# Kernel optimization log

Hardware: AMD Instinct MI355X
Metric: run time of the kernel (lower is better)

## Reference

```python
import jax, jax.numpy as jnp
import numpy as np

EMBED_DIM = 1024
NUM_HEADS = 16
HEAD_DIM = EMBED_DIM // NUM_HEADS  # 64, == n_wires of quantum kernel


def setup_inputs() -> dict:
    key = jax.random.key(0)
    k1, k2, k3, k4 = jax.random.split(key, 4)
    B, S = 2, 2048
    x = jax.random.normal(k1, (B, S, EMBED_DIM), dtype=jnp.float32)
    # fused QKV projection (no bias); PyTorch Linear stores [out, in]
    qkv_w = jax.random.normal(k2, (3 * EMBED_DIM, EMBED_DIM), dtype=jnp.float32) / np.sqrt(EMBED_DIM)
    out_w = jax.random.normal(k3, (EMBED_DIM, EMBED_DIM), dtype=jnp.float32) / np.sqrt(EMBED_DIM)
    # one trainable RY angle per wire (shared across q, k, v and all heads)
    qparams = jax.random.normal(k4, (HEAD_DIM,), dtype=jnp.float32)
    return {"x": x, "qkv_w": qkv_w, "out_w": out_w, "qparams": qparams}


def _split_heads(t):
    B, S, E = t.shape
    return t.reshape(B, S, NUM_HEADS, HEAD_DIM).transpose(0, 2, 1, 3)  # [B,H,S,D]


def _apply_quantum(t, qparams):
    # RX(x_i)|0> then RY(p_i), measure <Z> on each wire independently:
    # <Z> = cos(x_i) * cos(p_i) -- separable single-qubit circuit reduces to trig.
    return jnp.cos(t) * jnp.cos(qparams)  # broadcast over last dim D


def reference(x, qkv_w, out_w, qparams):
    B, S, E = x.shape
    proj = x @ qkv_w.T                       # [B,S,3E]
    q, k, v = jnp.split(proj, 3, axis=-1)    # each [B,S,E]
    q = _apply_quantum(_split_heads(q), qparams)  # [B,H,S,D]
    k = _apply_quantum(_split_heads(k), qparams)
    v = _apply_quantum(_split_heads(v), qparams)
    scores = jnp.einsum('bhqd,bhkd->bhqk', q, k) / np.sqrt(HEAD_DIM)
    attn = jax.nn.softmax(scores, axis=-1)   # dropout is identity in eval
    out = jnp.einsum('bhqk,bhkd->bhqd', attn, v)  # [B,H,S,D]
    out = out.transpose(0, 2, 1, 3).reshape(B, S, E)
    return out @ out_w.T
```

## Files before the change

kernel.cpp:

```cpp
#include <hip/hip_runtime.h>
#include <hip/hip_bf16.h>

#define S_LEN 2048
#define EMB 1024
#define NH 16
#define HD 64

typedef __attribute__((ext_vector_type(8))) __bf16 bf16x8;
typedef __attribute__((ext_vector_type(4))) float f32x4;
typedef __attribute__((ext_vector_type(16))) float f32x16;
typedef __attribute__((ext_vector_type(4))) unsigned int u32x4;

__device__ inline void gload_lds16(const void* g, void* l) {
    __builtin_amdgcn_global_load_lds(
        (const __attribute__((address_space(1))) unsigned int*)g,
        (__attribute__((address_space(3))) unsigned int*)l, 16, 0, 0);
}

__global__ __launch_bounds__(256) void cvt_all(
    const float* __restrict__ x, const float* __restrict__ wq,
    const float* __restrict__ wo,
    __hip_bfloat16* __restrict__ xb, __hip_bfloat16* __restrict__ wqb,
    __hip_bfloat16* __restrict__ wob)
{
    const long C_X = (long)4096 * 1024 / 4;
    const long C_WQ = (long)3072 * 1024 / 4;
    long c = (long)blockIdx.x * 256 + threadIdx.x;
    const float* in;
    __hip_bfloat16* out;
    if (c < C_X) { in = x; out = xb; }
    else if (c < C_X + C_WQ) { in = wq; out = wqb; c -= C_X; }
    else { in = wo; out = wob; c -= C_X + C_WQ; }
    long i = c * 4;
    float4 v = *(const float4*)(in + i);
    __hip_bfloat16 b0 = __float2bfloat16(v.x);
    __hip_bfloat16 b1 = __float2bfloat16(v.y);
    __hip_bfloat16 b2 = __float2bfloat16(v.z);
    __hip_bfloat16 b3 = __float2bfloat16(v.w);
    ushort4 o = {*(unsigned short*)&b0, *(unsigned short*)&b1,
                 *(unsigned short*)&b2, *(unsigned short*)&b3};
    *(ushort4*)(out + i) = o;
}

template <int EPI>
__global__ __launch_bounds__(256) void gemm_mfma(
    const __hip_bfloat16* __restrict__ A,
    const __hip_bfloat16* __restrict__ B,
    const float* __restrict__ qp,
    __hip_bfloat16* __restrict__ Q,
    __hip_bfloat16* __restrict__ Kp,
    __hip_bfloat16* __restrict__ Vt,
    float* __restrict__ C)
{
    const int Kd = 1024;
    __shared__ __align__(16) char Ash[128 * 128];
    __shared__ __align__(16) char Bsh[128 * 128];

    const int t  = threadIdx.x;
    const int w  = t >> 6;
    const int l  = t & 63;
    const int lg = l >> 4, lm = l & 15;
    const int wr = w >> 1, wc = w & 1;
    const int m0 = blockIdx.y * 128;
    const int n0 = blockIdx.x * 128;

    const int r8 = l >> 3;
    const int sb = ((l & 7) * 16) ^ (r8 << 4);
    const char* srcA = (const char*)A + ((long)(m0 + w * 32 + r8) * Kd) * 2 + sb;
    const char* srcB = (const char*)B + ((long)(n0 + w * 32 + r8) * Kd) * 2 + sb;

    f32x4 acc[4][4];
#pragma unroll
    for (int i = 0; i < 4; i++)
#pragma unroll
        for (int j = 0; j < 4; j++) acc[i][j] = (f32x4){0.f, 0.f, 0.f, 0.f};

    for (int kt = 0; kt < Kd * 2; kt += 128) {
#pragma unroll
        for (int j = 0; j < 4; j++) {
            gload_lds16(srcA + (long)j * 8 * Kd * 2 + kt, Ash + (w * 32 + j * 8) * 128);
            gload_lds16(srcB + (long)j * 8 * Kd * 2 + kt, Bsh + (w * 32 + j * 8) * 128);
        }
        __syncthreads();
#pragma unroll
        for (int kk = 0; kk < 2; kk++) {
            bf16x8 af[4], bfr[4];
            const int sw = (lm & 7) << 4;
            const int co = (kk * 64 + lg * 16);
#pragma unroll
            for (int mi = 0; mi < 4; mi++)
                af[mi] = *(const bf16x8*)(Ash + (wr * 64 + mi * 16 + lm) * 128 + (co ^ sw));
#pragma unroll
            for (int ni = 0; ni < 4; ni++)
                bfr[ni] = *(const bf16x8*)(Bsh + (wc * 64 + ni * 16 + lm) * 128 + (co ^ sw));
#pragma unroll
            for (int mi = 0; mi < 4; mi++)
#pragma unroll
                for (int ni = 0; ni < 4; ni++)
                    acc[mi][ni] = __builtin_amdgcn_mfma_f32_16x16x32_bf16(
                        af[mi], bfr[ni], acc[mi][ni], 0, 0, 0);
        }
        __syncthreads();
    }

    if constexpr (EPI == 0) {
        const int which = n0 >> 10;
        float cqp[4];
#pragma unroll
        for (int ni = 0; ni < 4; ni++)
            cqp[ni] = __cosf(qp[(wc * 64 + ni * 16 + lm) & 63]);

        if (which == 2) {
            char* T = (w < 2 ? Ash : Bsh) + (w & 1) * 8192;
#pragma unroll
            for (int mi = 0; mi < 4; mi++)
#pragma unroll
                for (int r = 0; r < 4; r++)
#pragma unroll
                    for (int ni = 0; ni < 4; ni++) {
                        int row = ni * 16 + lm;
                        int col = mi * 16 + lg * 4 + r;
                        float val = __cosf(acc[mi][ni][r]) * cqp[ni];
                        *(__hip_bfloat16*)(T + row * 128 +
                                           ((col * 2) ^ ((row & 7) << 4))) =
                            __float2bfloat16(val);
                    }
            const int h  = ((n0 & 1023) >> 6) + wc;
            const int bh = (m0 >> 11) * NH + h;
            const int sbase = (m0 & 2047) + wr * 64;
#pragma unroll
            for (int j = 0; j < 8; j++) {
                int c = j * 64 + l;
                int d = c >> 3;
                int sc = (c & 7) * 16;
                uint4 v = *(const uint4*)(T + d * 128 + (sc ^ ((d & 7) << 4)));
                *(uint4*)((char*)(Vt + ((long)bh * HD + d) * S_LEN + sbase) + sc) = v;
            }
        } else {
#pragma unroll
            for (int mi = 0; mi < 4; mi++) {
#pragma unroll
                for (int r = 0; r < 4; r++) {
                    int m = m0 + wr * 64 + mi * 16 + lg * 4 + r;
                    int b = m >> 11, s = m & 2047;
#pragma unroll
                    for (int ni = 0; ni < 4; ni++) {
                        int n = n0 + wc * 64 + ni * 16 + lm;
                        int d = n & 63;
                        int h = (n & 1023) >> 6;
                        int bh = b * NH + h;
                        float val = __cosf(acc[mi][ni][r]) * cqp[ni];
                        if (which == 0)
                            Q[((long)bh * S_LEN + s) * HD + d] =
                                __float2bfloat16(val * 0.180336880f);
                        else
                            Kp[((long)bh * S_LEN + s) * HD + d] = __float2bfloat16(val);
                    }
                }
            }
        }
    } else {
#pragma unroll
        for (int mi = 0; mi < 4; mi++)
#pragma unroll
            for (int r = 0; r < 4; r++) {
                int m = m0 + wr * 64 + mi * 16 + lg * 4 + r;
#pragma unroll
                for (int ni = 0; ni < 4; ni++) {
                    int n = n0 + wc * 64 + ni * 16 + lm;
                    C[(long)m * 1024 + n] = acc[mi][ni][r];
                }
            }
    }
}

__global__ __launch_bounds__(256, 4) void attn_mfma(
    const __hip_bfloat16* __restrict__ Q,
    const __hip_bfloat16* __restrict__ K,
    const __hip_bfloat16* __restrict__ Vt,
    __hip_bfloat16* __restrict__ O)
{
    __shared__ __align__(16) char Ksh[2][64 * 128];
    __shared__ __align__(16) char Vsh[2][64 * 128];

    const int L  = blockIdx.x;
    const int bh = (L & 7) + (L >> 8) * 8;
    const int q0 = ((L >> 3) & 31) * 64;
    const int b  = bh >> 4, h = bh & 15;
    const int t  = threadIdx.x;
    const int w  = t >> 6;
    const int qi = w & 1;
    const int ki = w >> 1;
    const int l  = t & 63;
    const int lo5 = l & 31;
    const int hi  = l >> 5;

    const char* Qr =
        (const char*)(Q + ((long)bh * S_LEN + q0 + qi * 32 + lo5) * HD);
    bf16x8 qf[4];
#pragma unroll
    for (int ks = 0; ks < 4; ks++)
        qf[ks] = *(const bf16x8*)(Qr + ks * 32 + hi * 16);

    f32x16 oacc[2] = {};
    float lsum = 0.f;
    const float EXPB = 11.54156033f;

    const char* Kgb = (const char*)(K + (long)bh * S_LEN * HD);
    const char* Vgb = (const char*)(Vt + (long)bh * HD * S_LEN);

    const int swb = ((l & 7) * 16) ^ (((l >> 3) & 7) << 4);
    const int row0 = w * 8 + (l >> 3);
    const char* Ksrc  = Kgb + (long)row0 * 128 + swb;
    const char* Vsrc0 = Vgb + (long)row0 * (S_LEN * 2) + swb;
    const char* Vsrc1 = Vgb + (long)(row0 + 32) * (S_LEN * 2) + swb;

    gload_lds16(Ksrc, Ksh[0] + w * 1024);
    gload_lds16(Ksrc + 32 * 128, Ksh[0] + w * 1024 + 4096);
    gload_lds16(Vsrc0, Vsh[0] + w * 1024);
    gload_lds16(Vsrc1, Vsh[0] + w * 1024 + 4096);

    const int swr = (lo5 & 7) << 4;
    int cur = 0;
    for (int kt = 0; kt < S_LEN; kt += 64) {
        __syncthreads();

        if (kt + 64 < S_LEN) {
            int nk = kt + 64;
            gload_lds16(Ksrc + (long)nk * 128, Ksh[cur ^ 1] + w * 1024);
            gload_lds16(Ksrc + (long)(nk + 32) * 128, Ksh[cur ^ 1] + w * 1024 + 4096);
            gload_lds16(Vsrc0 + (long)nk * 2, Vsh[cur ^ 1] + w * 1024);
            gload_lds16(Vsrc1 + (long)nk * 2, Vsh[cur ^ 1] + w * 1024 + 4096);
        }

        const char* Kc = Ksh[cur];
        const char* Vc = Vsh[cur];

        f32x16 s;
#pragma unroll
        for (int r = 0; r < 16; r++) s[r] = -EXPB;
        const char* Krow = Kc + (ki * 32 + lo5) * 128;
        __builtin_amdgcn_s_setprio(1);
#pragma unroll
        for (int ks = 0; ks < 4; ks++) {
            bf16x8 kf = *(const bf16x8*)(Krow + ((ks * 32 + hi * 16) ^ swr));
            s = __builtin_amdgcn_mfma_f32_32x32x16_bf16(kf, qf[ks], s, 0, 0, 0);
        }
        __builtin_amdgcn_s_setprio(0);

        float p[16];
#pragma unroll
        for (int r = 0; r < 16; r++) p[r] = __builtin_amdgcn_exp2f(s[r]);
#pragma unroll
        for (int r = 0; r < 16; r += 4)
            lsum += (p[r] + p[r + 1]) + (p[r + 2] + p[r + 3]);
        unsigned c0, c1, c2, c3, c4, c5, c6, c7;
        asm("v_cvt_pk_bf16_f32 %0, %1, %2" : "=v"(c0) : "v"(p[0]),  "v"(p[1]));
        asm("v_cvt_pk_bf16_f32 %0, %1, %2" : "=v"(c1) : "v"(p[2]),  "v"(p[3]));
        asm("v_cvt_pk_bf16_f32 %0, %1, %2" : "=v"(c2) : "v"(p[4]),  "v"(p[5]));
        asm("v_cvt_pk_bf16_f32 %0, %1, %2" : "=v"(c3) : "v"(p[6]),  "v"(p[7]));
        asm("v_cvt_pk_bf16_f32 %0, %1, %2" : "=v"(c4) : "v"(p[8]),  "v"(p[9]));
        asm("v_cvt_pk_bf16_f32 %0, %1, %2" : "=v"(c5) : "v"(p[10]), "v"(p[11]));
        asm("v_cvt_pk_bf16_f32 %0, %1, %2" : "=v"(c6) : "v"(p[12]), "v"(p[13]));
        asm("v_cvt_pk_bf16_f32 %0, %1, %2" : "=v"(c7) : "v"(p[14]), "v"(p[15]));
        asm("v_permlane32_swap_b32 %0, %1" : "+v"(c0), "+v"(c2));
        asm("v_permlane32_swap_b32 %0, %1" : "+v"(c1), "+v"(c3));
        asm("v_permlane32_swap_b32 %0, %1" : "+v"(c4), "+v"(c6));
        asm("v_permlane32_swap_b32 %0, %1" : "+v"(c5), "+v"(c7));
        u32x4 w0 = {c0, c1, c2, c3};
        u32x4 w1 = {c4, c5, c6, c7};
        bf16x8 pa0 = __builtin_bit_cast(bf16x8, w0);
        bf16x8 pa1 = __builtin_bit_cast(bf16x8, w1);

        __builtin_amdgcn_s_setprio(1);
#pragma unroll
        for (int db = 0; db < 2; db++) {
            const char* Vrow = Vc + (db * 32 + lo5) * 128;
            bf16x8 vf0 = *(const bf16x8*)(Vrow + ((ki * 64 + hi * 16) ^ swr));
            bf16x8 vf1 = *(const bf16x8*)(Vrow + ((ki * 64 + 32 + hi * 16) ^ swr));
            oacc[db] = __builtin_amdgcn_mfma_f32_32x32x16_bf16(pa0, vf0, oacc[db], 0, 0, 0);
            oacc[db] = __builtin_amdgcn_mfma_f32_32x32x16_bf16(pa1, vf1, oacc[db], 0, 0, 0);
        }
        __builtin_amdgcn_s_setprio(0);
        cur ^= 1;
    }

    lsum += __shfl_xor(lsum, 32, 64);
    __syncthreads();
    float* Osh = (float*)Ksh;
    float* Lsh = (float*)Vsh;
    if (ki == 1) {
        float* dst = Osh + qi * 2048;
#pragma unroll
        for (int db = 0; db < 2; db++)
#pragma unroll
            for (int r = 0; r < 16; r++)
                dst[(db * 16 + r) * 64 + l] = oacc[db][r];
        Lsh[qi * 64 + l] = lsum;
    }
    __syncthreads();
    if (ki == 0) {
        const float* src = Osh + qi * 2048;
#pragma unroll
        for (int db = 0; db < 2; db++)
#pragma unroll
            for (int r = 0; r < 16; r++)
                oacc[db][r] += src[(db * 16 + r) * 64 + l];
        lsum += Lsh[qi * 64 + l];
        float inv = 1.f / lsum;
#pragma unroll
        for (int r = 0; r < 16; r++) {
            int qr = (r & 3) + 8 * (r >> 2) + 4 * hi;
            float invr = __shfl(inv, qr, 32);
            int qrow = q0 + qi * 32 + qr;
            long base = ((long)b * S_LEN + qrow) * EMB + h * HD;
            O[base + lo5]      = __float2bfloat16(oacc[0][r] * invr);
            O[base + 32 + lo5] = __float2bfloat16(oacc[1][r] * invr);
        }
    }
}

extern "C" void kernel_launch(void* const* d_in, const int* in_sizes, int n_in,
                              void* d_out, int out_size, void* d_ws, size_t ws_size,
                              hipStream_t stream) {
    const float* x     = (const float*)d_in[0];
    const float* qkv_w = (const float*)d_in[1];
    const float* out_w = (const float*)d_in[2];
    const float* qp    = (const float*)d_in[3];
    float* out = (float*)d_out;

    const long NELEM = (long)2 * S_LEN * EMB;
    __hip_bfloat16* Q   = (__hip_bfloat16*)d_ws;
    __hip_bfloat16* K   = Q + NELEM;
    __hip_bfloat16* Vt  = K + NELEM;
    __hip_bfloat16* O   = Vt + NELEM;
    __hip_bfloat16* xb  = O + NELEM;
    __hip_bfloat16* wqb = xb + NELEM;
    __hip_bfloat16* wob = wqb + (long)3072 * 1024;

    dim3 blk(256);
    cvt_all<<<dim3(8192), blk, 0, stream>>>(x, qkv_w, out_w, xb, wqb, wob);
    gemm_mfma<0><<<dim3(3072 / 128, 4096 / 128), blk, 0, stream>>>(
        xb, wqb, qp, Q, K, Vt, nullptr);
    attn_mfma<<<dim3(1024), blk, 0, stream>>>(Q, K, Vt, O);
    gemm_mfma<1><<<dim3(1024 / 128, 4096 / 128), blk, 0, stream>>>(
        O, wob, nullptr, nullptr, nullptr, nullptr, out);
}
```

Baseline: 118.0 us.

## Split attention KV across wave pairs and swizzle GEMM block order

```diff
diff --git a/kernel.cpp b/kernel.cpp
--- a/kernel.cpp
+++ b/kernel.cpp
@@ -42,7 +42,7 @@
     *(ushort4*)(out + i) = o;
 }
 
-template <int EPI>
+template <int EPI, int BN, int NX, int CH>
 __global__ __launch_bounds__(256) void gemm_mfma(
     const __hip_bfloat16* __restrict__ A,
     const __hip_bfloat16* __restrict__ B,
@@ -53,50 +53,56 @@
     float* __restrict__ C)
 {
     const int Kd = 1024;
+    const int NI = BN / 32;
     __shared__ __align__(16) char Ash[128 * 128];
-    __shared__ __align__(16) char Bsh[128 * 128];
+    __shared__ __align__(16) char Bsh[BN * 128];
+
+    const int bid = blockIdx.x;
+    const int sw_ = (bid & 7) * CH + (bid >> 3);
+    const int m0 = (sw_ / NX) * 128;
+    const int n0 = (sw_ % NX) * BN;
 
     const int t  = threadIdx.x;
     const int w  = t >> 6;
     const int l  = t & 63;
     const int lg = l >> 4, lm = l & 15;
     const int wr = w >> 1, wc = w & 1;
-    const int m0 = blockIdx.y * 128;
-    const int n0 = blockIdx.x * 128;
 
     const int r8 = l >> 3;
     const int sb = ((l & 7) * 16) ^ (r8 << 4);
     const char* srcA = (const char*)A + ((long)(m0 + w * 32 + r8) * Kd) * 2 + sb;
-    const char* srcB = (const char*)B + ((long)(n0 + w * 32 + r8) * Kd) * 2 + sb;
-
-    f32x4 acc[4][4];
+    const char* srcB = (const char*)B + ((long)(n0 + w * (BN / 4) + r8) * Kd) * 2 + sb;
+
+    f32x4 acc[4][NI];
 #pragma unroll
     for (int i = 0; i < 4; i++)
 #pragma unroll
-        for (int j = 0; j < 4; j++) acc[i][j] = (f32x4){0.f, 0.f, 0.f, 0.f};
+        for (int j = 0; j < NI; j++) acc[i][j] = (f32x4){0.f, 0.f, 0.f, 0.f};
 
     for (int kt = 0; kt < Kd * 2; kt += 128) {
 #pragma unroll
-        for (int j = 0; j < 4; j++) {
+        for (int j = 0; j < 4; j++)
             gload_lds16(srcA + (long)j * 8 * Kd * 2 + kt, Ash + (w * 32 + j * 8) * 128);
-            gload_lds16(srcB + (long)j * 8 * Kd * 2 + kt, Bsh + (w * 32 + j * 8) * 128);
-        }
+#pragma unroll
+        for (int j = 0; j < NI; j++)
+            gload_lds16(srcB + (long)j * 8 * Kd * 2 + kt,
+                        Bsh + (w * (BN / 4) + j * 8) * 128);
         __syncthreads();
 #pragma unroll
         for (int kk = 0; kk < 2; kk++) {
-            bf16x8 af[4], bfr[4];
+            bf16x8 af[4], bfr[NI];
             const int sw = (lm & 7) << 4;
             const int co = (kk * 64 + lg * 16);
 #pragma unroll
             for (int mi = 0; mi < 4; mi++)
                 af[mi] = *(const bf16x8*)(Ash + (wr * 64 + mi * 16 + lm) * 128 + (co ^ sw));
 #pragma unroll
-            for (int ni = 0; ni < 4; ni++)
-                bfr[ni] = *(const bf16x8*)(Bsh + (wc * 64 + ni * 16 + lm) * 128 + (co ^ sw));
+            for (int ni = 0; ni < NI; ni++)
+                bfr[ni] = *(const bf16x8*)(Bsh + (wc * (BN / 2) + ni * 16 + lm) * 128 + (co ^ sw));
 #pragma unroll
             for (int mi = 0; mi < 4; mi++)
 #pragma unroll
-                for (int ni = 0; ni < 4; ni++)
+                for (int ni = 0; ni < NI; ni++)
                     acc[mi][ni] = __builtin_amdgcn_mfma_f32_16x16x32_bf16(
                         af[mi], bfr[ni], acc[mi][ni], 0, 0, 0);
         }
@@ -105,10 +111,10 @@
 
     if constexpr (EPI == 0) {
         const int which = n0 >> 10;
-        float cqp[4];
-#pragma unroll
-        for (int ni = 0; ni < 4; ni++)
-            cqp[ni] = __cosf(qp[(wc * 64 + ni * 16 + lm) & 63]);
+        float cqp[NI];
+#pragma unroll
+        for (int ni = 0; ni < NI; ni++)
+            cqp[ni] = __cosf(qp[(wc * (BN / 2) + ni * 16 + lm) & 63]);
 
         if (which == 2) {
             char* T = (w < 2 ? Ash : Bsh) + (w & 1) * 8192;
@@ -117,7 +123,7 @@
 #pragma unroll
                 for (int r = 0; r < 4; r++)
 #pragma unroll
-                    for (int ni = 0; ni < 4; ni++) {
+                    for (int ni = 0; ni < NI; ni++) {
                         int row = ni * 16 + lm;
                         int col = mi * 16 + lg * 4 + r;
                         float val = __cosf(acc[mi][ni][r]) * cqp[ni];
@@ -144,8 +150,8 @@
                     int m = m0 + wr * 64 + mi * 16 + lg * 4 + r;
                     int b = m >> 11, s = m & 2047;
 #pragma unroll
-                    for (int ni = 0; ni < 4; ni++) {
-                        int n = n0 + wc * 64 + ni * 16 + lm;
+                    for (int ni = 0; ni < NI; ni++) {
+                        int n = n0 + wc * (BN / 2) + ni * 16 + lm;
                         int d = n & 63;
                         int h = (n & 1023) >> 6;
                         int bh = b * NH + h;
@@ -166,22 +172,21 @@
             for (int r = 0; r < 4; r++) {
                 int m = m0 + wr * 64 + mi * 16 + lg * 4 + r;
 #pragma unroll
-                for (int ni = 0; ni < 4; ni++) {
-                    int n = n0 + wc * 64 + ni * 16 + lm;
+                for (int ni = 0; ni < NI; ni++) {
+                    int n = n0 + wc * (BN / 2) + ni * 16 + lm;
                     C[(long)m * 1024 + n] = acc[mi][ni][r];
                 }
             }
     }
 }
 
-__global__ __launch_bounds__(256, 4) void attn_mfma(
+__global__ __launch_bounds__(256, 2) void attn_mfma(
     const __hip_bfloat16* __restrict__ Q,
     const __hip_bfloat16* __restrict__ K,
     const __hip_bfloat16* __restrict__ Vt,
     __hip_bfloat16* __restrict__ O)
 {
-    __shared__ __align__(16) char Ksh[2][64 * 128];
-    __shared__ __align__(16) char Vsh[2][64 * 128];
+    __shared__ __align__(16) char smem[65536 + 1024];
 
     const int L  = blockIdx.x;
     const int bh = (L & 7) + (L >> 8) * 8;
@@ -189,21 +194,22 @@
     const int b  = bh >> 4, h = bh & 15;
     const int t  = threadIdx.x;
     const int w  = t >> 6;
-    const int qi = w & 1;
-    const int ki = w >> 1;
+    const int sp = w >> 1, kh = w & 1;
     const int l  = t & 63;
     const int lo5 = l & 31;
     const int hi  = l >> 5;
 
-    const char* Qr =
-        (const char*)(Q + ((long)bh * S_LEN + q0 + qi * 32 + lo5) * HD);
-    bf16x8 qf[4];
-#pragma unroll
-    for (int ks = 0; ks < 4; ks++)
-        qf[ks] = *(const bf16x8*)(Qr + ks * 32 + hi * 16);
-
-    f32x16 oacc[2] = {};
-    float lsum = 0.f;
+    bf16x8 qf[2][4];
+#pragma unroll
+    for (int g = 0; g < 2; g++) {
+        const char* Qr = (const char*)(Q + ((long)bh * S_LEN + q0 + g * 32 + lo5) * HD);
+#pragma unroll
+        for (int ks = 0; ks < 4; ks++)
+            qf[g][ks] = *(const bf16x8*)(Qr + ks * 32 + hi * 16);
+    }
+
+    f32x16 oacc[2][2] = {};
+    float lsum[2] = {0.f, 0.f};
     const float EXPB = 11.54156033f;
 
     const char* Kgb = (const char*)(K + (long)bh * S_LEN * HD);
@@ -215,108 +221,116 @@
     const char* Vsrc0 = Vgb + (long)row0 * (S_LEN * 2) + swb;
     const char* Vsrc1 = Vgb + (long)(row0 + 32) * (S_LEN * 2) + swb;
 
-    gload_lds16(Ksrc, Ksh[0] + w * 1024);
-    gload_lds16(Ksrc + 32 * 128, Ksh[0] + w * 1024 + 4096);
-    gload_lds16(Vsrc0, Vsh[0] + w * 1024);
-    gload_lds16(Vsrc1, Vsh[0] + w * 1024 + 4096);
+#define STAGE(buf, nk)                                                         \
+    do {                                                                       \
+        _Pragma("unroll") for (int sp2 = 0; sp2 < 2; sp2++) {                  \
+            char* Kd_ = smem + ((buf) * 2 + sp2) * 8192;                       \
+            char* Vd_ = smem + 32768 + ((buf) * 2 + sp2) * 8192;               \
+            int kb = (nk) + sp2 * 64;                                          \
+            gload_lds16(Ksrc + (long)kb * 128, Kd_ + w * 1024);                \
+            gload_lds16(Ksrc + (long)(kb + 32) * 128, Kd_ + w * 1024 + 4096);  \
+            gload_lds16(Vsrc0 + (long)kb * 2, Vd_ + w * 1024);                 \
+            gload_lds16(Vsrc1 + (long)kb * 2, Vd_ + w * 1024 + 4096);          \
+        }                                                                      \
+    } while (0)
+
+    STAGE(0, 0);
 
     const int swr = (lo5 & 7) << 4;
     int cur = 0;
-    for (int kt = 0; kt < S_LEN; kt += 64) {
+    for (int rd = 0; rd < 16; rd++) {
         __syncthreads();
 
-        if (kt + 64 < S_LEN) {
-            int nk = kt + 64;
-            gload_lds16(Ksrc + (long)nk * 128, Ksh[cur ^ 1] + w * 1024);
-            gload_lds16(Ksrc + (long)(nk + 32) * 128, Ksh[cur ^ 1] + w * 1024 + 4096);
-            gload_lds16(Vsrc0 + (long)nk * 2, Vsh[cur ^ 1] + w * 1024);
-            gload_lds16(Vsrc1 + (long)nk * 2, Vsh[cur ^ 1] + w * 1024 + 4096);
-        }
-
-        const char* Kc = Ksh[cur];
-        const char* Vc = Vsh[cur];
-
-        f32x16 s;
-#pragma unroll
-        for (int r = 0; r < 16; r++) s[r] = -EXPB;
-        const char* Krow = Kc + (ki * 32 + lo5) * 128;
+        if (rd < 15) STAGE(cur ^ 1, (rd + 1) * 128);
+
+        const char* Kc = smem + (cur * 2 + sp) * 8192;
+        const char* Vc = smem + 32768 + (cur * 2 + sp) * 8192;
+
+        f32x16 s0, s1;
+#pragma unroll
+        for (int r = 0; r < 16; r++) { s0[r] = -EXPB; s1[r] = -EXPB; }
+        const char* Krow = Kc + (kh * 32 + lo5) * 128;
         __builtin_amdgcn_s_setprio(1);
 #pragma unroll
         for (int ks = 0; ks < 4; ks++) {
             bf16x8 kf = *(const bf16x8*)(Krow + ((ks * 32 + hi * 16) ^ swr));
-            s = __builtin_amdgcn_mfma_f32_32x32x16_bf16(kf, qf[ks], s, 0, 0, 0);
+            s0 = __builtin_amdgcn_mfma_f32_32x32x16_bf16(kf, qf[0][ks], s0, 0, 0, 0);
+            s1 = __builtin_amdgcn_mfma_f32_32x32x16_bf16(kf, qf[1][ks], s1, 0, 0, 0);
         }
         __builtin_amdgcn_s_setprio(0);
 
-        float p[16];
-#pragma unroll
-        for (int r = 0; r < 16; r++) p[r] = __builtin_amdgcn_exp2f(s[r]);
-#pragma unroll
-        for (int r = 0; r < 16; r += 4)
-            lsum += (p[r] + p[r + 1]) + (p[r + 2] + p[r + 3]);
-        unsigned c0, c1, c2, c3, c4, c5, c6, c7;
-        asm("v_cvt_pk_bf16_f32 %0, %1, %2" : "=v"(c0) : "v"(p[0]),  "v"(p[1]));
-        asm("v_cvt_pk_bf16_f32 %0, %1, %2" : "=v"(c1) : "v"(p[2]),  "v"(p[3]));
-        asm("v_cvt_pk_bf16_f32 %0, %1, %2" : "=v"(c2) : "v"(p[4]),  "v"(p[5]));
-        asm("v_cvt_pk_bf16_f32 %0, %1, %2" : "=v"(c3) : "v"(p[6]),  "v"(p[7]));
-        asm("v_cvt_pk_bf16_f32 %0, %1, %2" : "=v"(c4) : "v"(p[8]),  "v"(p[9]));
-        asm("v_cvt_pk_bf16_f32 %0, %1, %2" : "=v"(c5) : "v"(p[10]), "v"(p[11]));
-        asm("v_cvt_pk_bf16_f32 %0, %1, %2" : "=v"(c6) : "v"(p[12]), "v"(p[13]));
-        asm("v_cvt_pk_bf16_f32 %0, %1, %2" : "=v"(c7) : "v"(p[14]), "v"(p[15]));
-        asm("v_permlane32_swap_b32 %0, %1" : "+v"(c0), "+v"(c2));
-        asm("v_permlane32_swap_b32 %0, %1" : "+v"(c1), "+v"(c3));
-        asm("v_permlane32_swap_b32 %0, %1" : "+v"(c4), "+v"(c6));
-        asm("v_permlane32_swap_b32 %0, %1" : "+v"(c5), "+v"(c7));
-        u32x4 w0 = {c0, c1, c2, c3};
-        u32x4 w1 = {c4, c5, c6, c7};
-        bf16x8 pa0 = __builtin_bit_cast(bf16x8, w0);
-        bf16x8 pa1 = __builtin_bit_cast(bf16x8, w1);
+        bf16x8 pa[2][2];
+#pragma unroll
+        for (int g = 0; g < 2; g++) {
+            const f32x16& sv = g ? s1 : s0;
+            float p[16];
+#pragma unroll
+            for (int r = 0; r < 16; r++) p[r] = __builtin_amdgcn_exp2f(sv[r]);
+#pragma unroll
+            for (int r = 0; r < 16; r += 4)
+                lsum[g] += (p[r] + p[r + 1]) + (p[r + 2] + p[r + 3]);
+            unsigned c0, c1, c2, c3, c4, c5, c6, c7;
+            asm("v_cvt_pk_bf16_f32 %0, %1, %2" : "=v"(c0) : "v"(p[0]),  "v"(p[1]));
+            asm("v_cvt_pk_bf16_f32 %0, %1, %2" : "=v"(c1) : "v"(p[2]),  "v"(p[3]));
+            asm("v_cvt_pk_bf16_f32 %0, %1, %2" : "=v"(c2) : "v"(p[4]),  "v"(p[5]));
+            asm("v_cvt_pk_bf16_f32 %0, %1, %2" : "=v"(c3) : "v"(p[6]),  "v"(p[7]));
+            asm("v_cvt_pk_bf16_f32 %0, %1, %2" : "=v"(c4) : "v"(p[8]),  "v"(p[9]));
+            asm("v_cvt_pk_bf16_f32 %0, %1, %2" : "=v"(c5) : "v"(p[10]), "v"(p[11]));
+            asm("v_cvt_pk_bf16_f32 %0, %1, %2" : "=v"(c6) : "v"(p[12]), "v"(p[13]));
+            asm("v_cvt_pk_bf16_f32 %0, %1, %2" : "=v"(c7) : "v"(p[14]), "v"(p[15]));
+            asm("v_permlane32_swap_b32 %0, %1" : "+v"(c0), "+v"(c2));
+            asm("v_permlane32_swap_b32 %0, %1" : "+v"(c1), "+v"(c3));
+            asm("v_permlane32_swap_b32 %0, %1" : "+v"(c4), "+v"(c6));
+            asm("v_permlane32_swap_b32 %0, %1" : "+v"(c5), "+v"(c7));
+            u32x4 w0 = {c0, c1, c2, c3};
+            u32x4 w1 = {c4, c5, c6, c7};
+            pa[g][0] = __builtin_bit_cast(bf16x8, w0);
+            pa[g][1] = __builtin_bit_cast(bf16x8, w1);
+        }
 
         __builtin_amdgcn_s_setprio(1);
 #pragma unroll
         for (int db = 0; db < 2; db++) {
             const char* Vrow = Vc + (db * 32 + lo5) * 128;
-            bf16x8 vf0 = *(const bf16x8*)(Vrow + ((ki * 64 + hi * 16) ^ swr));
-            bf16x8 vf1 = *(const bf16x8*)(Vrow + ((ki * 64 + 32 + hi * 16) ^ swr));
-            oacc[db] = __builtin_amdgcn_mfma_f32_32x32x16_bf16(pa0, vf0, oacc[db], 0, 0, 0);
-            oacc[db] = __builtin_amdgcn_mfma_f32_32x32x16_bf16(pa1, vf1, oacc[db], 0, 0, 0);
+            bf16x8 vf0 = *(const bf16x8*)(Vrow + ((kh * 64 + hi * 16) ^ swr));
+            bf16x8 vf1 = *(const bf16x8*)(Vrow + ((kh * 64 + 32 + hi * 16) ^ swr));
+            oacc[0][db] = __builtin_amdgcn_mfma_f32_32x32x16_bf16(pa[0][0], vf0, oacc[0][db], 0, 0, 0);
+            oacc[0][db] = __builtin_amdgcn_mfma_f32_32x32x16_bf16(pa[0][1], vf1, oacc[0][db], 0, 0, 0);
+            oacc[1][db] = __builtin_amdgcn_mfma_f32_32x32x16_bf16(pa[1][0], vf0, oacc[1][db], 0, 0, 0);
+            oacc[1][db] = __builtin_amdgcn_mfma_f32_32x32x16_bf16(pa[1][1], vf1, oacc[1][db], 0, 0, 0);
         }
         __builtin_amdgcn_s_setprio(0);
         cur ^= 1;
     }
-
-    lsum += __shfl_xor(lsum, 32, 64);
+#undef STAGE
+
+#pragma unroll
+    for (int g = 0; g < 2; g++) lsum[g] += __shfl_xor(lsum[g], 32, 64);
     __syncthreads();
-    float* Osh = (float*)Ksh;
-    float* Lsh = (float*)Vsh;
-    if (ki == 1) {
-        float* dst = Osh + qi * 2048;
+    float* Osh = (float*)smem;
+    float* Lsh = (float*)(smem + 65536);
+#pragma unroll
+    for (int g = 0; g < 2; g++)
 #pragma unroll
         for (int db = 0; db < 2; db++)
 #pragma unroll
-            for (int r = 0; r < 16; r++)
-                dst[(db * 16 + r) * 64 + l] = oacc[db][r];
-        Lsh[qi * 64 + l] = lsum;
+            for (int r = 0; r < 16; r++) {
+                int q = g * 32 + (r & 3) + 8 * (r >> 2) + 4 * hi;
+                Osh[w * 4096 + q * 64 + db * 32 + lo5] = oacc[g][db][r];
+            }
+    if (l < 32) {
+        Lsh[w * 64 + lo5]      = lsum[0];
+        Lsh[w * 64 + 32 + lo5] = lsum[1];
     }
     __syncthreads();
-    if (ki == 0) {
-        const float* src = Osh + qi * 2048;
-#pragma unroll
-        for (int db = 0; db < 2; db++)
-#pragma unroll
-            for (int r = 0; r < 16; r++)
-                oacc[db][r] += src[(db * 16 + r) * 64 + l];
-        lsum += Lsh[qi * 64 + l];
-        float inv = 1.f / lsum;
-#pragma unroll
-        for (int r = 0; r < 16; r++) {
-            int qr = (r & 3) + 8 * (r >> 2) + 4 * hi;
-            float invr = __shfl(inv, qr, 32);
-            int qrow = q0 + qi * 32 + qr;
-            long base = ((long)b * S_LEN + qrow) * EMB + h * HD;
-            O[base + lo5]      = __float2bfloat16(oacc[0][r] * invr);
-            O[base + 32 + lo5] = __float2bfloat16(oacc[1][r] * invr);
-        }
+#pragma unroll
+    for (int i = 0; i < 16; i++) {
+        int qh = w * 16 + i;
+        float Lq = Lsh[qh] + Lsh[64 + qh] + Lsh[128 + qh] + Lsh[192 + qh];
+        float v = Osh[qh * 64 + l] + Osh[4096 + qh * 64 + l] +
+                  Osh[8192 + qh * 64 + l] + Osh[12288 + qh * 64 + l];
+        O[((long)b * S_LEN + q0 + qh) * EMB + h * HD + l] =
+            __float2bfloat16(v * (1.f / Lq));
     }
 }
 
@@ -340,9 +354,9 @@
 
     dim3 blk(256);
     cvt_all<<<dim3(8192), blk, 0, stream>>>(x, qkv_w, out_w, xb, wqb, wob);
-    gemm_mfma<0><<<dim3(3072 / 128, 4096 / 128), blk, 0, stream>>>(
+    gemm_mfma<0, 128, 24, 96><<<dim3(768), blk, 0, stream>>>(
         xb, wqb, qp, Q, K, Vt, nullptr);
     attn_mfma<<<dim3(1024), blk, 0, stream>>>(Q, K, Vt, O);
-    gemm_mfma<1><<<dim3(1024 / 128, 4096 / 128), blk, 0, stream>>>(
+    gemm_mfma<1, 64, 16, 64><<<dim3(512), blk, 0, stream>>>(
         O, wob, nullptr, nullptr, nullptr, nullptr, out);
 }
```

Result: no change. 117.0 us (-0.9%).
